# Optimization experiments

Measured on AMD Instinct MI355X. Metric: run time of the kernel, lower is better.

The kernel has to match this reference:

```python
import jax, jax.numpy as jnp
import numpy as np

N_NODES = 100000
N_EDGES = 1600000
N_FEAT = 8
N_EFEAT = 4
STATE = 32  # node_state_size
N_GEN = 10000
ITERS = 3


def _fix_max(m):
    # TF unsorted_segment_max fills empty segments with dtype.min (finite)
    return jnp.where(jnp.isneginf(m), jnp.finfo(m.dtype).min, m)


def _fix_min(m):
    return jnp.where(jnp.isposinf(m), jnp.finfo(m.dtype).max, m)


def _l2_normalize(x, eps=1e-12):
    return x * jax.lax.rsqrt(jnp.maximum(jnp.sum(x * x, axis=-1, keepdims=True), eps))


def _dense_init(key, fan_in, fan_out):
    return jax.random.normal(key, (fan_in, fan_out), jnp.float32) * (1.0 / np.sqrt(fan_in))


def setup_inputs() -> dict:
    key = jax.random.key(0)
    ks = jax.random.split(key, 12)
    x = jax.random.normal(ks[0], (N_NODES, N_FEAT), jnp.float32)
    edge_weights = jax.random.uniform(ks[1], (N_EDGES, N_EFEAT), jnp.float32)
    edges = jax.random.randint(ks[2], (2, N_EDGES), 0, N_NODES)
    generators_nodes = jax.random.randint(ks[3], (N_GEN,), 0, N_NODES)
    # update_fn: 128 -> 256 -> 128 -> 32 (tanh)
    Wu1 = _dense_init(ks[4], 4 * STATE, 256); bu1 = jnp.zeros((256,), jnp.float32)
    Wu2 = _dense_init(ks[5], 256, 128);       bu2 = jnp.zeros((128,), jnp.float32)
    Wu3 = _dense_init(ks[6], 128, STATE);     bu3 = jnp.zeros((STATE,), jnp.float32)
    # readout: 32 -> 64 -> 32 -> 1 (tanh, tanh, linear)
    Wr1 = _dense_init(ks[7], STATE, 64);      br1 = jnp.zeros((64,), jnp.float32)
    Wr2 = _dense_init(ks[8], 64, 32);         br2 = jnp.zeros((32,), jnp.float32)
    Wr3 = _dense_init(ks[9], 32, 1);          br3 = jnp.zeros((1,), jnp.float32)
    return {"x": x, "edge_weights": edge_weights,
            "Wu1": Wu1, "bu1": bu1, "Wu2": Wu2, "bu2": bu2, "Wu3": Wu3, "bu3": bu3,
            "Wr1": Wr1, "br1": br1, "Wr2": Wr2, "br2": br2, "Wr3": Wr3, "br3": br3,
            "edges": edges, "generators_nodes": generators_nodes}


def reference(x, edge_weights, Wu1, bu1, Wu2, bu2, Wu3, bu3,
              Wr1, br1, Wr2, br2, Wr3, br3, edges, generators_nodes):
    n = x.shape[0]
    node_idx, nbr_idx = edges[0], edges[1]
    ones = jnp.ones((edge_weights.shape[0], 1), x.dtype)
    cnt = jnp.maximum(jax.ops.segment_sum(ones, node_idx, num_segments=n), 1.0)  # [n,1]

    # prepare(): edge-weight stats per destination node, concat with features, pad to STATE
    w_sum = jax.ops.segment_sum(edge_weights, node_idx, num_segments=n)
    w_mean = w_sum / cnt
    w_max = _fix_max(jax.ops.segment_max(edge_weights, node_idx, num_segments=n))
    w_min = _fix_min(jax.ops.segment_min(edge_weights, node_idx, num_segments=n))
    reps = jnp.concatenate([x, w_mean, w_max, w_min, w_sum], axis=1)  # [n, 24]
    reps = jnp.pad(reps, ((0, 0), (0, STATE - reps.shape[1])))        # [n, 32]

    for _ in range(ITERS):
        msgs = jnp.take(reps, nbr_idx, axis=0)  # gather neighbour states [E, 32]
        m_mean = jax.ops.segment_sum(msgs, node_idx, num_segments=n) / cnt
        m_max = _fix_max(jax.ops.segment_max(msgs, node_idx, num_segments=n))
        m_min = _fix_min(jax.ops.segment_min(msgs, node_idx, num_segments=n))
        h = jnp.concatenate([reps, m_mean, m_max, m_min], axis=1)  # [n, 128]
        h = jnp.tanh(h @ Wu1 + bu1)
        h = jnp.tanh(h @ Wu2 + bu2)
        h = jnp.tanh(h @ Wu3 + bu3)
        reps = _l2_normalize(h)

    reps = jnp.where(jnp.isnan(reps), jnp.zeros_like(reps), reps)
    g = jnp.take(reps, generators_nodes, axis=0)  # [n_gen, 32]
    g = jnp.tanh(g @ Wr1 + br1)
    g = jnp.tanh(g @ Wr2 + br2)
    values = g @ Wr3 + br3  # linear final activation
    return values.reshape(-1)
```

## Files before the change

### kernel.cpp

```cpp
#include <hip/hip_runtime.h>
#include <cfloat>
#include <cmath>


typedef _Float16 half_t;
typedef _Float16 half8 __attribute__((ext_vector_type(8)));
typedef _Float16 half4_t __attribute__((ext_vector_type(4)));
typedef _Float16 half2_t __attribute__((ext_vector_type(2)));
typedef float f32x4 __attribute__((ext_vector_type(4)));
typedef float f32x2 __attribute__((ext_vector_type(2)));

#define NPB 512
#define BIN_CAP 9216
#define IDXCAP 4352

__device__ __forceinline__ float fast_tanh(float x) {
    float e = __builtin_amdgcn_exp2f(x * 2.8853900817779268f);
    return 1.0f - 2.0f * __builtin_amdgcn_rcpf(1.0f + e);
}

__device__ __forceinline__ half_t cvt_clamp(float v) {
    return (half_t)fminf(fmaxf(v, -60000.f), 60000.f);
}

__device__ __forceinline__ half2_t h2shfl_xor(half2_t v, int mask) {
    int i = __builtin_bit_cast(int, v);
    i = __shfl_xor(i, mask);
    return __builtin_bit_cast(half2_t, i);
}

__global__ __launch_bounds__(256) void k_binA(
    const int* __restrict__ dst, const int* __restrict__ src,
    const float4* __restrict__ ew4,
    int* __restrict__ binCnt, int4* __restrict__ staged, int E, int nbins) {
    __shared__ int cnt[256], base[256], cur[256];
    int t = threadIdx.x;
    cnt[t] = 0;
    cur[t] = 0;
    __syncthreads();
    int e0 = blockIdx.x * 8192;
#pragma unroll 4
    for (int i = 0; i < 32; ++i) {
        int e = e0 + i * 256 + t;
        if (e < E) atomicAdd(&cnt[dst[e] >> 9], 1);
    }
    __syncthreads();
    if (t < nbins && cnt[t] > 0) base[t] = atomicAdd(&binCnt[t], cnt[t]);
    __syncthreads();
#pragma unroll 4
    for (int i = 0; i < 32; ++i) {
        int e = e0 + i * 256 + t;
        if (e < E) {
            int d = dst[e];
            int b = d >> 9;
            int j = base[b] + atomicAdd(&cur[b], 1);
            if (j < BIN_CAP) {
                float4 w = ew4[e];
                half2_t lo = {(half_t)w.x, (half_t)w.y};
                half2_t hi = {(half_t)w.z, (half_t)w.w};
                staged[(size_t)b * BIN_CAP + j] =
                    make_int4(src[e], d & (NPB - 1),
                              __builtin_bit_cast(int, lo),
                              __builtin_bit_cast(int, hi));
            }
        }
    }
}

__global__ void k_scanN(const int* __restrict__ binCnt, int* __restrict__ binStart,
                        int* __restrict__ row_start, int nbins, int n, int E) {
    __shared__ int sh[256];
    int t = threadIdx.x;
    int v = (t < nbins) ? binCnt[t] : 0;
    sh[t] = v;
    __syncthreads();
    for (int s = 1; s < 256; s <<= 1) {
        int u = (t >= s) ? sh[t - s] : 0;
        __syncthreads();
        sh[t] += u;
        __syncthreads();
    }
    if (t < nbins) binStart[t] = sh[t] - v;
    if (t == 0) row_start[n] = E;
}

__global__ __launch_bounds__(512) void k_binB(
    const int* __restrict__ binCnt, const int* __restrict__ binStart,
    const int4* __restrict__ staged, const float* __restrict__ x,
    int* __restrict__ row_start, int* __restrict__ snbr, int2* __restrict__ sew,
    half_t* __restrict__ reps, int n) {
    __shared__ int deg[NPB], cur[NPB], rsl[NPB];
    int t = threadIdx.x;
    int bin = blockIdx.x;
    int cntE = min(binCnt[bin], BIN_CAP);
    int pbase = binStart[bin];
    const int4* st = staged + (size_t)bin * BIN_CAP;

    deg[t] = 0;
    cur[t] = 0;
    __syncthreads();

    for (int i = t; i < cntE; i += 512)
        atomicAdd(&deg[st[i].y], 1);
    __syncthreads();

    int own = deg[t];
    for (int s = 1; s < NPB; s <<= 1) {
        int u = (t >= s) ? deg[t - s] : 0;
        __syncthreads();
        deg[t] += u;
        __syncthreads();
    }
    int excl = deg[t] - own;
    rsl[t] = pbase + excl;
    int node = bin * NPB + t;
    if (node < n) row_start[node] = pbase + excl;
    __syncthreads();

    for (int i = t; i < cntE; i += 512) {
        int4 v = st[i];
        int p = rsl[v.y] + atomicAdd(&cur[v.y], 1);
        snbr[p] = v.x;
        sew[p] = make_int2(v.z, v.w);
    }
    __syncthreads();

    if (node < n) {
        int base = rsl[t];
        float s0 = 0.f, s1 = 0.f, s2 = 0.f, s3 = 0.f;
        half2_t mxlo = {(half_t)-65504.f, (half_t)-65504.f};
        half2_t mxhi = mxlo;
        half2_t mnlo = {(half_t)65504.f, (half_t)65504.f};
        half2_t mnhi = mnlo;
#pragma unroll 2
        for (int k = 0; k < own; ++k) {
            int2 e = sew[base + k];
            half2_t lo = __builtin_bit_cast(half2_t, e.x);
            half2_t hi = __builtin_bit_cast(half2_t, e.y);
            s0 += (float)lo[0];
            s1 += (float)lo[1];
            s2 += (float)hi[0];
            s3 += (float)hi[1];
            mxlo = __builtin_elementwise_max(mxlo, lo);
            mxhi = __builtin_elementwise_max(mxhi, hi);
            mnlo = __builtin_elementwise_min(mnlo, lo);
            mnhi = __builtin_elementwise_min(mnhi, hi);
        }
        float cnt = fmaxf((float)own, 1.0f);
        float rc = __builtin_amdgcn_rcpf(cnt);
        float mx0, mx1, mx2, mx3, mn0, mn1, mn2, mn3;
        if (own == 0) {
            mx0 = mx1 = mx2 = mx3 = -FLT_MAX;
            mn0 = mn1 = mn2 = mn3 = FLT_MAX;
        } else {
            mx0 = (float)mxlo[0]; mx1 = (float)mxlo[1];
            mx2 = (float)mxhi[0]; mx3 = (float)mxhi[1];
            mn0 = (float)mnlo[0]; mn1 = (float)mnlo[1];
            mn2 = (float)mnhi[0]; mn3 = (float)mnhi[1];
        }
        const float4* x4 = reinterpret_cast<const float4*>(x);
        float4 x0 = x4[node * 2 + 0], x1 = x4[node * 2 + 1];
        half_t* o = &reps[(size_t)node * 32];
        half8 c0 = {cvt_clamp(x0.x), cvt_clamp(x0.y), cvt_clamp(x0.z), cvt_clamp(x0.w),
                    cvt_clamp(x1.x), cvt_clamp(x1.y), cvt_clamp(x1.z), cvt_clamp(x1.w)};
        half8 c1 = {cvt_clamp(s0 * rc), cvt_clamp(s1 * rc), cvt_clamp(s2 * rc), cvt_clamp(s3 * rc),
                    cvt_clamp(mx0), cvt_clamp(mx1), cvt_clamp(mx2), cvt_clamp(mx3)};
        half8 c2 = {cvt_clamp(mn0), cvt_clamp(mn1), cvt_clamp(mn2), cvt_clamp(mn3),
                    cvt_clamp(s0), cvt_clamp(s1), cvt_clamp(s2), cvt_clamp(s3)};
        half8 c3 = {(half_t)0.f, (half_t)0.f, (half_t)0.f, (half_t)0.f,
                    (half_t)0.f, (half_t)0.f, (half_t)0.f, (half_t)0.f};
        *(half8*)&o[0] = c0;
        *(half8*)&o[8] = c1;
        *(half8*)&o[16] = c2;
        *(half8*)&o[24] = c3;
    }
}

__global__ void k_wprep(const float* __restrict__ Wu1, const float* __restrict__ Wu2,
                        const float* __restrict__ Wu3, half_t* __restrict__ Wt1,
                        half_t* __restrict__ Wt2, half_t* __restrict__ Wt3) {
    int i = blockIdx.x * 256 + threadIdx.x;
    if (i < 32768) {
        int nrow = i >> 7, k = i & 127;
        Wt1[i] = (half_t)Wu1[k * 256 + nrow];
    } else if (i < 65536) {
        int j = i - 32768;
        int nrow = j >> 8, k = j & 255;
        Wt2[j] = (half_t)Wu2[k * 128 + nrow];
    } else if (i < 69632) {
        int j = i - 65536;
        int nrow = j >> 7, k = j & 127;
        Wt3[j] = (half_t)Wu3[k * 32 + nrow];
    }
}

#define MFMA16(a, b, c) __builtin_amdgcn_mfma_f32_16x16x32_f16((a), (b), (c), 0, 0, 0)

__global__ __launch_bounds__(512, 6) void k_mlp(
    const half_t* __restrict__ reps_in,
    const int* __restrict__ row_start, const int* __restrict__ snbr,
    const int* __restrict__ nlist, int nlen,
    const half_t* __restrict__ Wt1, const half_t* __restrict__ Wt2,
    const half_t* __restrict__ Wt3,
    const float* __restrict__ bu1, const float* __restrict__ bu2,
    const float* __restrict__ bu3,
    half_t* __restrict__ reps_out, int n) {
    __shared__ half_t sH[64 * 136];
    __shared__ half_t sh1c[64 * 136];
    __shared__ int sDeg[64], sPerm[64], sNode[64];
    int* sIdx = (int*)sh1c;

    const int tid = threadIdx.x;
    const int w   = tid >> 6;
    const int l15 = tid & 15;
    const int lk  = (tid & 63) >> 4;
    const int node0 = blockIdx.x * 64;

    if (tid < 64) {
        int node;
        if (nlist) {
            int li = node0 + tid;
            node = (li < nlen) ? nlist[li] : -1;
        } else {
            node = node0 + tid;
        }
        if ((unsigned)node >= (unsigned)n) node = -1;
        sNode[tid] = node;
        sDeg[tid] = (node >= 0) ? (row_start[node + 1] - row_start[node]) : 0;
    }
    const int nodeEnd = min(node0 + 64, n);
    int d0blk = 0;
    bool lds_ok = false;
    if (!nlist && node0 < n) {
        d0blk = row_start[node0];
        int ecnt = row_start[nodeEnd] - d0blk;
        lds_ok = (ecnt <= IDXCAP);
        if (lds_ok) {
            for (int i = tid; i < ecnt; i += 512)
                sIdx[i] = __builtin_nontemporal_load(&snbr[d0blk + i]);
        }
    }
    __syncthreads();
    if (tid < 64) {
        int dg = sDeg[tid];
        int rank = 0;
#pragma unroll
        for (int j = 0; j < 64; ++j) {
            int dj = sDeg[j];
            rank += (dj > dg) || (dj == dg && j < tid);
        }
        sPerm[rank] = tid;
    }
    __syncthreads();

    {
        const int sg = tid >> 4;
        const int l  = tid & 15;
        const int nb = l >> 2;
        const int ch = l & 3;

        for (int i = 0; i < 2; ++i) {
            int nl = sPerm[i * 32 + sg];
            int node = sNode[nl];
            half8 ownrow;
            if (nb == 0 && node >= 0)
                ownrow = *(const half8*)&reps_in[(size_t)node * 32 + ch * 8];
            f32x2 s2[4];
            half2_t mx2[4], mn2[4];
#pragma unroll
            for (int f = 0; f < 4; ++f) {
                s2[f] = (f32x2){0.f, 0.f};
                mx2[f] = (half2_t){(half_t)-65504.f, (half_t)-65504.f};
                mn2[f] = (half2_t){(half_t)65504.f, (half_t)65504.f};
            }
            int d0 = 0, d1 = 0;
            if (node >= 0) { d0 = row_start[node]; d1 = row_start[node + 1]; }

            for (int e = d0; e < d1; e += 16) {
                int e0 = e + nb, e1 = e + 4 + nb, e2 = e + 8 + nb, e3 = e + 12 + nb;
                f32x2 m0 = (e0 < d1) ? (f32x2){1.f, 1.f} : (f32x2){0.f, 0.f};
                f32x2 m1 = (e1 < d1) ? (f32x2){1.f, 1.f} : (f32x2){0.f, 0.f};
                f32x2 m2 = (e2 < d1) ? (f32x2){1.f, 1.f} : (f32x2){0.f, 0.f};
                f32x2 m3 = (e3 < d1) ? (f32x2){1.f, 1.f} : (f32x2){0.f, 0.f};
                int ii0, ii1, ii2, ii3;
                if (lds_ok) {
                    ii0 = sIdx[min(e0, d1 - 1) - d0blk];
                    ii1 = sIdx[min(e1, d1 - 1) - d0blk];
                    ii2 = sIdx[min(e2, d1 - 1) - d0blk];
                    ii3 = sIdx[min(e3, d1 - 1) - d0blk];
                } else {
                    ii0 = snbr[min(e0, d1 - 1)];
                    ii1 = snbr[min(e1, d1 - 1)];
                    ii2 = snbr[min(e2, d1 - 1)];
                    ii3 = snbr[min(e3, d1 - 1)];
                }
                half8 r0 = *(const half8*)&reps_in[(size_t)ii0 * 32 + ch * 8];
                half8 r1 = *(const half8*)&reps_in[(size_t)ii1 * 32 + ch * 8];
                half8 r2 = *(const half8*)&reps_in[(size_t)ii2 * 32 + ch * 8];
                half8 r3 = *(const half8*)&reps_in[(size_t)ii3 * 32 + ch * 8];
#pragma unroll
                for (int f = 0; f < 4; ++f) {
                    half2_t a0 = (half2_t){r0[2 * f], r0[2 * f + 1]};
                    half2_t a1 = (half2_t){r1[2 * f], r1[2 * f + 1]};
                    half2_t a2 = (half2_t){r2[2 * f], r2[2 * f + 1]};
                    half2_t a3 = (half2_t){r3[2 * f], r3[2 * f + 1]};
                    mx2[f] = __builtin_elementwise_max(
                        __builtin_elementwise_max(mx2[f], a0),
                        __builtin_elementwise_max(a1,
                            __builtin_elementwise_max(a2, a3)));
                    mn2[f] = __builtin_elementwise_min(
                        __builtin_elementwise_min(mn2[f], a0),
                        __builtin_elementwise_min(a1,
                            __builtin_elementwise_min(a2, a3)));
                    f32x2 v0 = {(float)a0[0], (float)a0[1]};
                    f32x2 v1 = {(float)a1[0], (float)a1[1]};
                    f32x2 v2 = {(float)a2[0], (float)a2[1]};
                    f32x2 v3 = {(float)a3[0], (float)a3[1]};
                    s2[f] = v0 * m0 + s2[f];
                    s2[f] = v1 * m1 + s2[f];
                    s2[f] = v2 * m2 + s2[f];
                    s2[f] = v3 * m3 + s2[f];
                }
            }
#pragma unroll
            for (int f = 0; f < 4; ++f) {
                s2[f][0] += __shfl_xor(s2[f][0], 4);
                s2[f][1] += __shfl_xor(s2[f][1], 4);
                s2[f][0] += __shfl_xor(s2[f][0], 8);
                s2[f][1] += __shfl_xor(s2[f][1], 8);
                mx2[f] = __builtin_elementwise_max(mx2[f], h2shfl_xor(mx2[f], 4));
                mx2[f] = __builtin_elementwise_max(mx2[f], h2shfl_xor(mx2[f], 8));
                mn2[f] = __builtin_elementwise_min(mn2[f], h2shfl_xor(mn2[f], 4));
                mn2[f] = __builtin_elementwise_min(mn2[f], h2shfl_xor(mn2[f], 8));
            }
            float cnt = fmaxf((float)(d1 - d0), 1.f);
            half8 o;
            if (nb == 0) {
                if (node >= 0) {
                    o = ownrow;
                } else {
#pragma unroll
                    for (int f = 0; f < 8; ++f) o[f] = (half_t)0.f;
                }
            } else if (nb == 1) {
                float rc = __builtin_amdgcn_rcpf(cnt);
#pragma unroll
                for (int f = 0; f < 4; ++f) {
                    o[2 * f]     = cvt_clamp(s2[f][0] * rc);
                    o[2 * f + 1] = cvt_clamp(s2[f][1] * rc);
                }
            } else if (nb == 2) {
#pragma unroll
                for (int f = 0; f < 4; ++f) {
                    o[2 * f]     = cvt_clamp((float)mx2[f][0]);
                    o[2 * f + 1] = cvt_clamp((float)mx2[f][1]);
                }
            } else {
#pragma unroll
                for (int f = 0; f < 4; ++f) {
                    o[2 * f]     = cvt_clamp((float)mn2[f][0]);
                    o[2 * f + 1] = cvt_clamp((float)mn2[f][1]);
                }
            }
            *(half8*)&sH[nl * 136 + l * 8] = o;
        }
    }
    __syncthreads();

    f32x4 acc2[4] = {{0.f, 0.f, 0.f, 0.f}, {0.f, 0.f, 0.f, 0.f},
                     {0.f, 0.f, 0.f, 0.f}, {0.f, 0.f, 0.f, 0.f}};
#pragma unroll
    for (int c = 0; c < 2; ++c) {
        {
            half8 a[4];
#pragma unroll
            for (int ks = 0; ks < 4; ++ks)
                a[ks] = *(const half8*)&Wt1[(c * 128 + w * 16 + l15) * 128 + ks * 32 + lk * 8];
            f32x4 bv = *(const f32x4*)&bu1[c * 128 + w * 16 + lk * 4];
#pragma unroll
            for (int nt = 0; nt < 4; ++nt) {
                const half_t* hrow = &sH[(nt * 16 + l15) * 136 + lk * 8];
                half8 b0 = *(const half8*)&hrow[0];
                half8 b1 = *(const half8*)&hrow[32];
                half8 b2 = *(const half8*)&hrow[64];
                half8 b3 = *(const half8*)&hrow[96];
                f32x4 acc = {0.f, 0.f, 0.f, 0.f};
                acc = MFMA16(a[0], b0, acc);
                acc = MFMA16(a[1], b1, acc);
                acc = MFMA16(a[2], b2, acc);
                acc = MFMA16(a[3], b3, acc);
                half4_t o;
#pragma unroll
                for (int r = 0; r < 4; ++r)
                    o[r] = (half_t)fast_tanh(acc[r] + bv[r]);
                *(half4_t*)&sh1c[(nt * 16 + l15) * 136 + w * 16 + lk * 4] = o;
            }
        }
        __syncthreads();
        {
            half8 a[4];
#pragma unroll
            for (int ks = 0; ks < 4; ++ks)
                a[ks] = *(const half8*)&Wt2[(w * 16 + l15) * 256 + c * 128 + ks * 32 + lk * 8];
#pragma unroll
            for (int nt = 0; nt < 4; ++nt) {
#pragma unroll
                for (int ks = 0; ks < 4; ++ks) {
                    half8 b = *(const half8*)&sh1c[(nt * 16 + l15) * 136 + ks * 32 + lk * 8];
                    acc2[nt] = MFMA16(a[ks], b, acc2[nt]);
                }
            }
        }
        __syncthreads();
    }

    {
        f32x4 bv = *(const f32x4*)&bu2[w * 16 + lk * 4];
#pragma unroll
        for (int nt = 0; nt < 4; ++nt) {
            half4_t o;
#pragma unroll
            for (int r = 0; r < 4; ++r)
                o[r] = (half_t)fast_tanh(acc2[nt][r] + bv[r]);
            *(half4_t*)&sH[(nt * 16 + l15) * 136 + w * 16 + lk * 4] = o;
        }
    }
    __syncthreads();

    if (w < 4) {
        half8 a0[4], a1[4], b[4];
#pragma unroll
        for (int ks = 0; ks < 4; ++ks) {
            a0[ks] = *(const half8*)&Wt3[l15 * 128 + ks * 32 + lk * 8];
            a1[ks] = *(const half8*)&Wt3[(16 + l15) * 128 + ks * 32 + lk * 8];
            b[ks]  = *(const half8*)&sH[(w * 16 + l15) * 136 + ks * 32 + lk * 8];
        }
        f32x4 acc0 = {0.f, 0.f, 0.f, 0.f}, acc1 = {0.f, 0.f, 0.f, 0.f};
#pragma unroll
        for (int ks = 0; ks < 4; ++ks) {
            acc0 = MFMA16(a0[ks], b[ks], acc0);
            acc1 = MFMA16(a1[ks], b[ks], acc1);
        }
        f32x4 bv0 = *(const f32x4*)&bu3[lk * 4];
        f32x4 bv1 = *(const f32x4*)&bu3[16 + lk * 4];
        float v0[4], v1[4];
        float ss = 0.f;
#pragma unroll
        for (int r = 0; r < 4; ++r) {
            v0[r] = fast_tanh(acc0[r] + bv0[r]);
            v1[r] = fast_tanh(acc1[r] + bv1[r]);
            ss += v0[r] * v0[r] + v1[r] * v1[r];
        }
        ss += __shfl_xor(ss, 16);
        ss += __shfl_xor(ss, 32);
        float sc = rsqrtf(fmaxf(ss, 1e-12f));
        int node = sNode[w * 16 + l15];
        if (node >= 0) {
            half4_t o0, o1;
#pragma unroll
            for (int r = 0; r < 4; ++r) {
                o0[r] = (half_t)(v0[r] * sc);
                o1[r] = (half_t)(v1[r] * sc);
            }
            *(half4_t*)&reps_out[(size_t)node * 32 + lk * 4] = o0;
            *(half4_t*)&reps_out[(size_t)node * 32 + 16 + lk * 4] = o1;
        }
    }
}

__global__ __launch_bounds__(256) void k_readout(
    const half_t* __restrict__ reps, const int* __restrict__ gen,
    const float* __restrict__ Wr1, const float* __restrict__ br1,
    const float* __restrict__ Wr2, const float* __restrict__ br2,
    const float* __restrict__ Wr3, const float* __restrict__ br3,
    float* __restrict__ out, int ngen) {
    __shared__ float sW1[32 * 64];
    __shared__ float sW2[64 * 32];
    __shared__ float sb1[64];
    __shared__ float sb2[32];
    __shared__ float sW3r[32];
    __shared__ float sb3;
    int tid = threadIdx.x;
    for (int i = tid; i < 2048; i += 256) sW1[i] = Wr1[i];
    for (int i = tid; i < 2048; i += 256) sW2[i] = Wr2[i];
    if (tid < 64) sb1[tid] = br1[tid];
    if (tid < 32) sb2[tid] = br2[tid];
    if (tid < 32) sW3r[tid] = Wr3[tid];
    if (tid == 0) sb3 = br3[0];
    __syncthreads();
    int ig = blockIdx.x * 256 + tid;
    if (ig >= ngen) return;
    int node = gen[ig];
    float g[32];
#pragma unroll
    for (int q = 0; q < 4; ++q) {
        half8 v = *(const half8*)&reps[(size_t)node * 32 + q * 8];
#pragma unroll
        for (int r = 0; r < 8; ++r) {
            float f = (float)v[r];
            g[q * 8 + r] = (f != f) ? 0.f : f;
        }
    }
    float a[64];
#pragma unroll
    for (int o = 0; o < 64; ++o) {
        float acc = sb1[o];
#pragma unroll
        for (int k = 0; k < 32; ++k) acc = fmaf(g[k], sW1[k * 64 + o], acc);
        a[o] = fast_tanh(acc);
    }
    float b[32];
#pragma unroll
    for (int o = 0; o < 32; ++o) {
        float acc = sb2[o];
#pragma unroll
        for (int k = 0; k < 64; ++k) acc = fmaf(a[k], sW2[k * 32 + o], acc);
        b[o] = fast_tanh(acc);
    }
    float acc = sb3;
#pragma unroll
    for (int k = 0; k < 32; ++k) acc = fmaf(b[k], sW3r[k], acc);
    out[ig] = acc;
}

extern "C" void kernel_launch(void* const* d_in, const int* in_sizes, int n_in,
                              void* d_out, int out_size, void* d_ws, size_t ws_size,
                              hipStream_t stream) {
    const float* x   = (const float*)d_in[0];
    const float* ew  = (const float*)d_in[1];
    const float* Wu1 = (const float*)d_in[2];
    const float* bu1 = (const float*)d_in[3];
    const float* Wu2 = (const float*)d_in[4];
    const float* bu2 = (const float*)d_in[5];
    const float* Wu3 = (const float*)d_in[6];
    const float* bu3 = (const float*)d_in[7];
    const float* Wr1 = (const float*)d_in[8];
    const float* br1 = (const float*)d_in[9];
    const float* Wr2 = (const float*)d_in[10];
    const float* br2 = (const float*)d_in[11];
    const float* Wr3 = (const float*)d_in[12];
    const float* br3 = (const float*)d_in[13];
    const int* edges = (const int*)d_in[14];
    const int* gen   = (const int*)d_in[15];

    const int n    = in_sizes[0] / 8;
    const int E    = in_sizes[1] / 4;
    const int ngen = in_sizes[15];
    const int* dst = edges;
    const int* src = edges + E;
    float* out = (float*)d_out;

    const int nblk  = (n + 63) / 64;
    const int npad  = nblk * 64;
    const int nbins = (n + NPB - 1) / NPB;

    char* ws = (char*)d_ws;
    size_t off = 0;
    auto alloc = [&](size_t bytes) -> char* {
        char* p = ws + off;
        off = (off + bytes + 255) & ~(size_t)255;
        return p;
    };
    int* row_start = (int*)alloc((size_t)(n + 1) * 4);
    int* binCnt    = (int*)alloc(256 * 4);
    int* binStart  = (int*)alloc(256 * 4);
    int* snbr      = (int*)alloc((size_t)E * 4);
    int2* sew      = (int2*)alloc((size_t)E * 8);
    half_t* repsA  = (half_t*)alloc((size_t)npad * 32 * 2);
    half_t* repsB  = (half_t*)alloc((size_t)npad * 32 * 2);
    half_t* Wt1    = (half_t*)alloc(32768 * 2);
    half_t* Wt2    = (half_t*)alloc(32768 * 2);
    half_t* Wt3    = (half_t*)alloc(4096 * 2);
    int4* staged   = (int4*)alloc((size_t)nbins * BIN_CAP * 16);

    hipMemsetAsync(binCnt, 0, 256 * 4, stream);
    int nblkA = (E + 8191) / 8192;
    k_binA<<<nblkA, 256, 0, stream>>>(dst, src, (const float4*)ew, binCnt, staged, E, nbins);
    k_scanN<<<1, 256, 0, stream>>>(binCnt, binStart, row_start, nbins, n, E);
    k_binB<<<nbins, 512, 0, stream>>>(binCnt, binStart, staged, x,
                                      row_start, snbr, sew, repsA, n);
    k_wprep<<<272, 256, 0, stream>>>(Wu1, Wu2, Wu3, Wt1, Wt2, Wt3);

    k_mlp<<<nblk, 512, 0, stream>>>(repsA, row_start, snbr, nullptr, 0,
                                    Wt1, Wt2, Wt3, bu1, bu2, bu3, repsB, n);
    k_mlp<<<nblk, 512, 0, stream>>>(repsB, row_start, snbr, nullptr, 0,
                                    Wt1, Wt2, Wt3, bu1, bu2, bu3, repsA, n);
    int nblk3 = (ngen + 63) / 64;
    k_mlp<<<nblk3, 512, 0, stream>>>(repsA, row_start, snbr, gen, ngen,
                                     Wt1, Wt2, Wt3, bu1, bu2, bu3, repsB, n);

    k_readout<<<(ngen + 255) / 256, 256, 0, stream>>>(repsB, gen, Wr1, br1, Wr2, br2,
                                                      Wr3, br3, out, ngen);
}
```

Before: 261.7 us.

## Fold bin-count scan into binB, widen binB to 1024 threads, shrink binA chunks

Removes the separate single-block scan kernel by having every binB block redundantly scan the 256 bin counts in shared memory, which saves one launch and a dependency bubble. binB now runs 1024 threads so the two passes over staged edges use twice the threads, while the per-node statistics still use the first 512. binA processes 4096 edges per block instead of 8192, giving more blocks and more global atomics on binCnt. The redundant scan adds a few syncs per block, and the larger block may reduce how many blocks fit per CU.

```diff
diff --git a/kernel.cpp b/kernel.cpp
--- a/kernel.cpp
+++ b/kernel.cpp
@@ -38,9 +38,9 @@
     cnt[t] = 0;
     cur[t] = 0;
     __syncthreads();
-    int e0 = blockIdx.x * 8192;
+    int e0 = blockIdx.x * 4096;
 #pragma unroll 4
-    for (int i = 0; i < 32; ++i) {
+    for (int i = 0; i < 16; ++i) {
         int e = e0 + i * 256 + t;
         if (e < E) atomicAdd(&cnt[dst[e] >> 9], 1);
     }
@@ -48,7 +48,7 @@
     if (t < nbins && cnt[t] > 0) base[t] = atomicAdd(&binCnt[t], cnt[t]);
     __syncthreads();
 #pragma unroll 4
-    for (int i = 0; i < 32; ++i) {
+    for (int i = 0; i < 16; ++i) {
         int e = e0 + i * 256 + t;
         if (e < E) {
             int d = dst[e];
@@ -67,57 +67,51 @@
     }
 }
 
-__global__ void k_scanN(const int* __restrict__ binCnt, int* __restrict__ binStart,
-                        int* __restrict__ row_start, int nbins, int n, int E) {
-    __shared__ int sh[256];
-    int t = threadIdx.x;
-    int v = (t < nbins) ? binCnt[t] : 0;
-    sh[t] = v;
-    __syncthreads();
-    for (int s = 1; s < 256; s <<= 1) {
-        int u = (t >= s) ? sh[t - s] : 0;
-        __syncthreads();
-        sh[t] += u;
-        __syncthreads();
-    }
-    if (t < nbins) binStart[t] = sh[t] - v;
-    if (t == 0) row_start[n] = E;
-}
-
-__global__ __launch_bounds__(512) void k_binB(
-    const int* __restrict__ binCnt, const int* __restrict__ binStart,
+__global__ __launch_bounds__(1024) void k_binB(
+    const int* __restrict__ binCnt,
     const int4* __restrict__ staged, const float* __restrict__ x,
     int* __restrict__ row_start, int* __restrict__ snbr, int2* __restrict__ sew,
-    half_t* __restrict__ reps, int n) {
+    half_t* __restrict__ reps, int n, int E, int nbins) {
     __shared__ int deg[NPB], cur[NPB], rsl[NPB];
+    __shared__ int sBC[256];
     int t = threadIdx.x;
     int bin = blockIdx.x;
+
+    if (t < 256) sBC[t] = (t < nbins) ? binCnt[t] : 0;
+    if (t < NPB) { deg[t] = 0; cur[t] = 0; }
+    __syncthreads();
+    for (int s = 1; s < 256; s <<= 1) {
+        int u = (t < 256 && t >= s) ? sBC[t - s] : 0;
+        __syncthreads();
+        if (t < 256) sBC[t] += u;
+        __syncthreads();
+    }
+    int pbase = (bin > 0) ? sBC[bin - 1] : 0;
+    if (bin == 0 && t == 0) row_start[n] = E;
+
     int cntE = min(binCnt[bin], BIN_CAP);
-    int pbase = binStart[bin];
     const int4* st = staged + (size_t)bin * BIN_CAP;
 
-    deg[t] = 0;
-    cur[t] = 0;
-    __syncthreads();
-
-    for (int i = t; i < cntE; i += 512)
+    for (int i = t; i < cntE; i += 1024)
         atomicAdd(&deg[st[i].y], 1);
     __syncthreads();
 
-    int own = deg[t];
+    int own = (t < NPB) ? deg[t] : 0;
     for (int s = 1; s < NPB; s <<= 1) {
-        int u = (t >= s) ? deg[t - s] : 0;
+        int u = (t < NPB && t >= s) ? deg[t - s] : 0;
         __syncthreads();
-        deg[t] += u;
+        if (t < NPB) deg[t] += u;
         __syncthreads();
     }
-    int excl = deg[t] - own;
-    rsl[t] = pbase + excl;
     int node = bin * NPB + t;
-    if (node < n) row_start[node] = pbase + excl;
-    __syncthreads();
-
-    for (int i = t; i < cntE; i += 512) {
+    if (t < NPB) {
+        int excl = deg[t] - own;
+        rsl[t] = pbase + excl;
+        if (node < n) row_start[node] = pbase + excl;
+    }
+    __syncthreads();
+
+    for (int i = t; i < cntE; i += 1024) {
         int4 v = st[i];
         int p = rsl[v.y] + atomicAdd(&cur[v.y], 1);
         snbr[p] = v.x;
@@ -125,7 +119,7 @@
     }
     __syncthreads();
 
-    if (node < n) {
+    if (t < NPB && node < n) {
         int base = rsl[t];
         float s0 = 0.f, s1 = 0.f, s2 = 0.f, s3 = 0.f;
         half2_t mxlo = {(half_t)-65504.f, (half_t)-65504.f};
@@ -563,7 +557,6 @@
     };
     int* row_start = (int*)alloc((size_t)(n + 1) * 4);
     int* binCnt    = (int*)alloc(256 * 4);
-    int* binStart  = (int*)alloc(256 * 4);
     int* snbr      = (int*)alloc((size_t)E * 4);
     int2* sew      = (int2*)alloc((size_t)E * 8);
     half_t* repsA  = (half_t*)alloc((size_t)npad * 32 * 2);
@@ -574,11 +567,10 @@
     int4* staged   = (int4*)alloc((size_t)nbins * BIN_CAP * 16);
 
     hipMemsetAsync(binCnt, 0, 256 * 4, stream);
-    int nblkA = (E + 8191) / 8192;
+    int nblkA = (E + 4095) / 4096;
     k_binA<<<nblkA, 256, 0, stream>>>(dst, src, (const float4*)ew, binCnt, staged, E, nbins);
-    k_scanN<<<1, 256, 0, stream>>>(binCnt, binStart, row_start, nbins, n, E);
-    k_binB<<<nbins, 512, 0, stream>>>(binCnt, binStart, staged, x,
-                                      row_start, snbr, sew, repsA, n);
+    k_binB<<<nbins, 1024, 0, stream>>>(binCnt, staged, x,
+                                       row_start, snbr, sew, repsA, n, E, nbins);
     k_wprep<<<272, 256, 0, stream>>>(Wu1, Wu2, Wu3, Wt1, Wt2, Wt3);
 
     k_mlp<<<nblk, 512, 0, stream>>>(repsA, row_start, snbr, nullptr, 0,
```

After: 248.9 us. 1.05x faster.
